# Performance work log

Hardware: AMD Instinct MI355X
Metric: run time of the kernel (lower is better)

## Reference

```python
import jax, jax.numpy as jnp
from jax import lax
import numpy as np

E = 16          # n_routed_experts
H = 2048        # hidden_size
I = 1408        # moe_intermediate_size
T = 2048        # tokens
K = 6           # top_k


def setup_inputs() -> dict:
    key = jax.random.key(0)
    k1, k2, k3, k4, k5 = jax.random.split(key, 5)
    hidden_states = jax.random.normal(k1, (T, H), dtype=jnp.float32)
    top_k_index = jax.random.randint(k2, (T, K), 0, E)
    top_k_weights = jax.random.uniform(k3, (T, K), dtype=jnp.float32)
    gate_up_proj = jax.random.normal(k4, (E, 2 * I, H), dtype=jnp.float32) * 0.02
    down_proj = jax.random.normal(k5, (E, H, I), dtype=jnp.float32) * 0.02
    return {
        "hidden_states": hidden_states,
        "top_k_index": top_k_index,
        "top_k_weights": top_k_weights,
        "gate_up_proj": gate_up_proj,
        "down_proj": down_proj,
    }


def reference(hidden_states, top_k_index, top_k_weights, gate_up_proj, down_proj):
    # combine[t, e] = sum over k-slots of top_k_weights[t, k] where top_k_index[t, k] == e
    # (scatter-add handles duplicate expert picks identically to index_add_).
    n_tok = hidden_states.shape[0]
    n_exp = gate_up_proj.shape[0]
    combine = jnp.zeros((n_tok, n_exp), hidden_states.dtype)
    combine = combine.at[jnp.arange(n_tok)[:, None], top_k_index].add(top_k_weights)

    def expert_step(acc, params):
        gu, dn, c_e = params  # gu: [2I, H], dn: [H, I], c_e: [n_tok]
        gate, up = jnp.split(hidden_states @ gu.T, 2, axis=-1)  # each [n_tok, I]
        y = (jax.nn.silu(gate) * up) @ dn.T                     # [n_tok, H]
        return acc + y * c_e[:, None], None

    out, _ = lax.scan(
        expert_step,
        jnp.zeros_like(hidden_states),
        (gate_up_proj, down_proj, combine.T),
    )
    return out
```

## Files before the change

### kernel.cpp

```cpp
#include <hip/hip_runtime.h>
#include <hip/hip_bf16.h>
#include <cstdint>

#define T_TOK 2048
#define HD 2048
#define ID 1408
#define NE 16
#define TOPK 6

#define BM 256
#define BN 64
#define BK 64

typedef __bf16 bf16x8 __attribute__((ext_vector_type(8)));
typedef float f32x4 __attribute__((ext_vector_type(4)));

typedef const __attribute__((address_space(1))) void* gas1_t;
typedef __attribute__((address_space(3))) void* las3_t;
#define GLDS16(g, l) __builtin_amdgcn_global_load_lds((gas1_t)(g), (las3_t)(l), 16, 0, 0)


__global__ void k_combine(const int* __restrict__ idx, const float* __restrict__ w,
                          float* __restrict__ combine) {
    int t = blockIdx.x * blockDim.x + threadIdx.x;
    if (t >= T_TOK) return;
    int ie[TOPK];
    float fw[TOPK];
#pragma unroll
    for (int k = 0; k < TOPK; k++) { ie[k] = idx[t * TOPK + k]; fw[k] = w[t * TOPK + k]; }
#pragma unroll
    for (int e = 0; e < NE; e++) {
        float s = 0.f;
#pragma unroll
        for (int k = 0; k < TOPK; k++) if (ie[k] == e) s += fw[k];
        combine[t * NE + e] = s;
    }
}

__global__ void k_lists(const float* __restrict__ combine, int* __restrict__ counts,
                        int* __restrict__ tok, float* __restrict__ wts) {
    int t = blockIdx.x * blockDim.x + threadIdx.x;
    if (t >= T_TOK) return;
    for (int e = 0; e < NE; e++) {
        float c = combine[t * NE + e];
        if (c != 0.0f) {
            int p = atomicAdd(&counts[e], 1);
            tok[e * T_TOK + p] = t;
            wts[e * T_TOK + p] = c;
        }
    }
}

__global__ void k_cvt(const float* __restrict__ x, __bf16* __restrict__ xb) {
    int i = (blockIdx.x * 256 + threadIdx.x) * 8;
    float4 a = *(const float4*)(x + i);
    float4 b = *(const float4*)(x + i + 4);
    bf16x8 o;
    o[0] = (__bf16)a.x; o[1] = (__bf16)a.y; o[2] = (__bf16)a.z; o[3] = (__bf16)a.w;
    o[4] = (__bf16)b.x; o[5] = (__bf16)b.y; o[6] = (__bf16)b.z; o[7] = (__bf16)b.w;
    *(bf16x8*)(xb + i) = o;
}


__device__ __forceinline__ int swz(int row, int cb) {
    return row * 128 + (cb ^ ((row & 7) << 4));
}

__device__ __forceinline__ bf16x8 ldfrag(const __bf16* base, int row, int cb) {
    return *(const bf16x8*)((const char*)base + swz(row, cb));
}

__device__ __forceinline__ void stage8v(char* lds, int row, int cb, float4 f0, float4 f1) {
    bf16x8 o;
    o[0] = (__bf16)f0.x; o[1] = (__bf16)f0.y; o[2] = (__bf16)f0.z; o[3] = (__bf16)f0.w;
    o[4] = (__bf16)f1.x; o[5] = (__bf16)f1.y; o[6] = (__bf16)f1.z; o[7] = (__bf16)f1.w;
    *(bf16x8*)(lds + swz(row, cb)) = o;
}


__global__ __launch_bounds__(512, 4) void k_gemm1(
    const __bf16* __restrict__ Xb, const float* __restrict__ gup,
    const int* __restrict__ counts, const int* __restrict__ tok,
    __bf16* __restrict__ act) {
    int x = blockIdx.x;
    int e = x / 22;
    int n0 = (x % 22) * BN;
    int cnt = counts[e];
    int m0 = blockIdx.y * BM;
    if (m0 >= cnt) return;

    __shared__ __align__(16) __bf16 sA[2][BM * BK];
    __shared__ __align__(16) __bf16 sBg[BN * BK];
    __shared__ __align__(16) __bf16 sBu[BN * BK];

    int tid = threadIdx.x;
    int lane = tid & 63;
    int wid = tid >> 6;

    const __bf16* pA[4];
    int csw = ((lane & 7) ^ ((lane >> 3) & 7)) * 8;
#pragma unroll
    for (int j = 0; j < 4; j++) {
        int r = 32 * wid + 8 * j + (lane >> 3);
        int g = m0 + r;
        if (g >= cnt) g = cnt - 1;
        pA[j] = Xb + (size_t)tok[e * T_TOK + g] * HD + csw;
    }

    int br = tid >> 3, bc = tid & 7;
    const float* gbase = gup + (size_t)e * (2 * ID) * HD;
    const float* bgSrc = gbase + (size_t)(n0 + br) * HD + bc * 8;
    const float* buSrc = gbase + (size_t)(ID + n0 + br) * HD + bc * 8;

    int wm = wid >> 1, wn = wid & 1;
    int l15 = lane & 15, lh = lane >> 4;

    f32x4 accg[4][2] = {};
    f32x4 accu[4][2] = {};

    float4 g0 = ((const float4*)bgSrc)[0], g1 = ((const float4*)bgSrc)[1];
    float4 u0 = ((const float4*)buSrc)[0], u1 = ((const float4*)buSrc)[1];
#pragma unroll
    for (int j = 0; j < 4; j++)
        GLDS16(pA[j], &sA[0][(32 * wid + 8 * j) * BK]);
    __syncthreads();

    const int NT = HD / BK;
    for (int k = 0; k < NT; k++) {
        int cur = k & 1;
        stage8v((char*)sBg, br, bc * 16, g0, g1);
        stage8v((char*)sBu, br, bc * 16, u0, u1);
        __syncthreads();

        if (k + 1 < NT) {
            int k0 = (k + 1) * BK;
#pragma unroll
            for (int j = 0; j < 4; j++)
                GLDS16(pA[j] + k0, &sA[cur ^ 1][(32 * wid + 8 * j) * BK]);
            const float* bg = bgSrc + k0;
            const float* bu = buSrc + k0;
            g0 = ((const float4*)bg)[0]; g1 = ((const float4*)bg)[1];
            u0 = ((const float4*)bu)[0]; u1 = ((const float4*)bu)[1];
        }

        const __bf16* sAc = sA[cur];
#pragma unroll
        for (int kk = 0; kk < 2; kk++) {
            int cb = kk * 64 + lh * 16;
            bf16x8 a[4];
#pragma unroll
            for (int fm = 0; fm < 4; fm++)
                a[fm] = ldfrag(sAc, wm * 64 + fm * 16 + l15, cb);
#pragma unroll
            for (int fn = 0; fn < 2; fn++) {
                bf16x8 bg = ldfrag(sBg, wn * 32 + fn * 16 + l15, cb);
                bf16x8 bu = ldfrag(sBu, wn * 32 + fn * 16 + l15, cb);
#pragma unroll
                for (int fm = 0; fm < 4; fm++) {
                    accg[fm][fn] = __builtin_amdgcn_mfma_f32_16x16x32_bf16(a[fm], bg, accg[fm][fn], 0, 0, 0);
                    accu[fm][fn] = __builtin_amdgcn_mfma_f32_16x16x32_bf16(a[fm], bu, accu[fm][fn], 0, 0, 0);
                }
            }
        }
        __syncthreads();
    }

#pragma unroll
    for (int fm = 0; fm < 4; fm++) {
#pragma unroll
        for (int fn = 0; fn < 2; fn++) {
#pragma unroll
            for (int j = 0; j < 4; j++) {
                int mloc = wm * 64 + fm * 16 + lh * 4 + j;
                int g = m0 + mloc;
                if (g < cnt) {
                    float gv = accg[fm][fn][j];
                    float uv = accu[fm][fn][j];
                    float sv = gv * (1.0f / (1.0f + __expf(-gv)));
                    int n = n0 + wn * 32 + fn * 16 + l15;
                    act[((size_t)e * T_TOK + g) * ID + n] = (__bf16)(sv * uv);
                }
            }
        }
    }
}


__global__ __launch_bounds__(512, 4) void k_gemm2(
    const __bf16* __restrict__ act, const float* __restrict__ dn,
    const int* __restrict__ counts, const int* __restrict__ tok,
    const float* __restrict__ wts, float* __restrict__ out) {
    int x = blockIdx.x;
    int e = x >> 5;
    int n0 = (x & 31) * BN;
    int cnt = counts[e];
    int m0 = blockIdx.y * BM;
    if (m0 >= cnt) return;

    __shared__ __align__(16) __bf16 sA[2][BM * BK];
    __shared__ __align__(16) __bf16 sB[BN * BK];
    __shared__ int tokLds[BM];
    __shared__ float wtLds[BM];

    int tid = threadIdx.x;
    if (tid < BM) {
        int g = m0 + tid;
        bool v = g < cnt;
        tokLds[tid] = v ? tok[e * T_TOK + g] : 0;
        wtLds[tid] = v ? wts[e * T_TOK + g] : 0.f;
    }

    int lane = tid & 63;
    int wid = tid >> 6;

    const __bf16* pA[4];
    int csw = ((lane & 7) ^ ((lane >> 3) & 7)) * 8;
#pragma unroll
    for (int j = 0; j < 4; j++) {
        int r = 32 * wid + 8 * j + (lane >> 3);
        pA[j] = act + ((size_t)e * T_TOK + m0 + r) * ID + csw;
    }

    int br = tid >> 3, bc = tid & 7;
    const float* bSrc = dn + (size_t)e * HD * ID + (size_t)(n0 + br) * ID + bc * 8;

    int wm = wid >> 1, wn = wid & 1;
    int l15 = lane & 15, lh = lane >> 4;

    f32x4 acc[4][2] = {};

    float4 b0 = ((const float4*)bSrc)[0], b1 = ((const float4*)bSrc)[1];
#pragma unroll
    for (int j = 0; j < 4; j++)
        GLDS16(pA[j], &sA[0][(32 * wid + 8 * j) * BK]);
    __syncthreads();

    const int NT = ID / BK;
    for (int k = 0; k < NT; k++) {
        int cur = k & 1;
        stage8v((char*)sB, br, bc * 16, b0, b1);
        __syncthreads();

        if (k + 1 < NT) {
            int k0 = (k + 1) * BK;
#pragma unroll
            for (int j = 0; j < 4; j++)
                GLDS16(pA[j] + k0, &sA[cur ^ 1][(32 * wid + 8 * j) * BK]);
            const float* bs = bSrc + k0;
            b0 = ((const float4*)bs)[0]; b1 = ((const float4*)bs)[1];
        }

        const __bf16* sAc = sA[cur];
#pragma unroll
        for (int kk = 0; kk < 2; kk++) {
            int cb = kk * 64 + lh * 16;
            bf16x8 a[4];
#pragma unroll
            for (int fm = 0; fm < 4; fm++)
                a[fm] = ldfrag(sAc, wm * 64 + fm * 16 + l15, cb);
#pragma unroll
            for (int fn = 0; fn < 2; fn++) {
                bf16x8 b = ldfrag(sB, wn * 32 + fn * 16 + l15, cb);
#pragma unroll
                for (int fm = 0; fm < 4; fm++)
                    acc[fm][fn] = __builtin_amdgcn_mfma_f32_16x16x32_bf16(a[fm], b, acc[fm][fn], 0, 0, 0);
            }
        }
        __syncthreads();
    }

#pragma unroll
    for (int fm = 0; fm < 4; fm++) {
#pragma unroll
        for (int fn = 0; fn < 2; fn++) {
#pragma unroll
            for (int j = 0; j < 4; j++) {
                int mloc = wm * 64 + fm * 16 + lh * 4 + j;
                int g = m0 + mloc;
                if (g < cnt) {
                    float v = acc[fm][fn][j] * wtLds[mloc];
                    int n = n0 + wn * 32 + fn * 16 + l15;
                    atomicAdd(&out[(size_t)tokLds[mloc] * HD + n], v);
                }
            }
        }
    }
}


extern "C" void kernel_launch(void* const* d_in, const int* in_sizes, int n_in,
                              void* d_out, int out_size, void* d_ws, size_t ws_size,
                              hipStream_t stream) {
    const float* hs = (const float*)d_in[0];
    const int* tki = (const int*)d_in[1];
    const float* tkw = (const float*)d_in[2];
    const float* gup = (const float*)d_in[3];
    const float* dnp = (const float*)d_in[4];
    float* out = (float*)d_out;

    char* p = (char*)d_ws;
    int* counts = (int*)p;      p += 256;
    float* combine = (float*)p; p += (size_t)T_TOK * NE * 4;
    int* tok = (int*)p;         p += (size_t)NE * T_TOK * 4;
    float* wts = (float*)p;     p += (size_t)NE * T_TOK * 4;
    __bf16* Xb = (__bf16*)p;    p += (size_t)T_TOK * HD * 2;
    __bf16* act = (__bf16*)p;

    hipMemsetAsync(counts, 0, 256, stream);
    hipMemsetAsync(d_out, 0, (size_t)T_TOK * HD * 4, stream);
    k_combine<<<T_TOK / 256, 256, 0, stream>>>(tki, tkw, combine);
    k_lists<<<T_TOK / 256, 256, 0, stream>>>(combine, counts, tok, wts);
    k_cvt<<<(T_TOK * HD / 8) / 256, 256, 0, stream>>>(hs, Xb);
    k_gemm1<<<dim3(22 * NE, T_TOK / BM), 512, 0, stream>>>(Xb, gup, counts, tok, act);
    k_gemm2<<<dim3(32 * NE, T_TOK / BM), 512, 0, stream>>>(act, dnp, counts, tok, wts, out);
}
```

Before: 471.0 us.

## Double-buffer B tiles in LDS to drop one barrier per K step

Both GEMM kernels now keep two LDS buffers for the fp32-to-bf16 staged weight tile, written for the next iteration after the MFMA loop. This removes the mid-iteration __syncthreads, leaving one barrier per K step, and hides the global B load latency behind the compute. The extra LDS raises shared memory use, and k_gemm1's launch bound drops from 4 to 2 blocks per CU, which may reduce occupancy but frees registers.

```diff
diff --git a/kernel.cpp b/kernel.cpp
--- a/kernel.cpp
+++ b/kernel.cpp
@@ -78,7 +78,7 @@
 }
 
 
-__global__ __launch_bounds__(512, 4) void k_gemm1(
+__global__ __launch_bounds__(512, 2) void k_gemm1(
     const __bf16* __restrict__ Xb, const float* __restrict__ gup,
     const int* __restrict__ counts, const int* __restrict__ tok,
     __bf16* __restrict__ act) {
@@ -90,8 +90,8 @@
     if (m0 >= cnt) return;
 
     __shared__ __align__(16) __bf16 sA[2][BM * BK];
-    __shared__ __align__(16) __bf16 sBg[BN * BK];
-    __shared__ __align__(16) __bf16 sBu[BN * BK];
+    __shared__ __align__(16) __bf16 sBg[2][BN * BK];
+    __shared__ __align__(16) __bf16 sBu[2][BN * BK];
 
     int tid = threadIdx.x;
     int lane = tid & 63;
@@ -118,25 +118,28 @@
     f32x4 accg[4][2] = {};
     f32x4 accu[4][2] = {};
 
-    float4 g0 = ((const float4*)bgSrc)[0], g1 = ((const float4*)bgSrc)[1];
-    float4 u0 = ((const float4*)buSrc)[0], u1 = ((const float4*)buSrc)[1];
-#pragma unroll
-    for (int j = 0; j < 4; j++)
-        GLDS16(pA[j], &sA[0][(32 * wid + 8 * j) * BK]);
+    const int NT = HD / BK;
+
+    {
+        float4 g0 = ((const float4*)bgSrc)[0], g1 = ((const float4*)bgSrc)[1];
+        float4 u0 = ((const float4*)buSrc)[0], u1 = ((const float4*)buSrc)[1];
+#pragma unroll
+        for (int j = 0; j < 4; j++)
+            GLDS16(pA[j], &sA[0][(32 * wid + 8 * j) * BK]);
+        stage8v((char*)sBg[0], br, bc * 16, g0, g1);
+        stage8v((char*)sBu[0], br, bc * 16, u0, u1);
+    }
     __syncthreads();
 
-    const int NT = HD / BK;
     for (int k = 0; k < NT; k++) {
-        int cur = k & 1;
-        stage8v((char*)sBg, br, bc * 16, g0, g1);
-        stage8v((char*)sBu, br, bc * 16, u0, u1);
-        __syncthreads();
-
-        if (k + 1 < NT) {
+        int cur = k & 1, nxt = cur ^ 1;
+        bool pf = (k + 1 < NT);
+        float4 g0, g1, u0, u1;
+        if (pf) {
             int k0 = (k + 1) * BK;
 #pragma unroll
             for (int j = 0; j < 4; j++)
-                GLDS16(pA[j] + k0, &sA[cur ^ 1][(32 * wid + 8 * j) * BK]);
+                GLDS16(pA[j] + k0, &sA[nxt][(32 * wid + 8 * j) * BK]);
             const float* bg = bgSrc + k0;
             const float* bu = buSrc + k0;
             g0 = ((const float4*)bg)[0]; g1 = ((const float4*)bg)[1];
@@ -144,6 +147,8 @@
         }
 
         const __bf16* sAc = sA[cur];
+        const __bf16* sBgc = sBg[cur];
+        const __bf16* sBuc = sBu[cur];
 #pragma unroll
         for (int kk = 0; kk < 2; kk++) {
             int cb = kk * 64 + lh * 16;
@@ -153,14 +158,19 @@
                 a[fm] = ldfrag(sAc, wm * 64 + fm * 16 + l15, cb);
 #pragma unroll
             for (int fn = 0; fn < 2; fn++) {
-                bf16x8 bg = ldfrag(sBg, wn * 32 + fn * 16 + l15, cb);
-                bf16x8 bu = ldfrag(sBu, wn * 32 + fn * 16 + l15, cb);
+                bf16x8 bg = ldfrag(sBgc, wn * 32 + fn * 16 + l15, cb);
+                bf16x8 bu = ldfrag(sBuc, wn * 32 + fn * 16 + l15, cb);
 #pragma unroll
                 for (int fm = 0; fm < 4; fm++) {
                     accg[fm][fn] = __builtin_amdgcn_mfma_f32_16x16x32_bf16(a[fm], bg, accg[fm][fn], 0, 0, 0);
                     accu[fm][fn] = __builtin_amdgcn_mfma_f32_16x16x32_bf16(a[fm], bu, accu[fm][fn], 0, 0, 0);
                 }
             }
+        }
+
+        if (pf) {
+            stage8v((char*)sBg[nxt], br, bc * 16, g0, g1);
+            stage8v((char*)sBu[nxt], br, bc * 16, u0, u1);
         }
         __syncthreads();
     }
@@ -198,7 +208,7 @@
     if (m0 >= cnt) return;
 
     __shared__ __align__(16) __bf16 sA[2][BM * BK];
-    __shared__ __align__(16) __bf16 sB[BN * BK];
+    __shared__ __align__(16) __bf16 sB[2][BN * BK];
     __shared__ int tokLds[BM];
     __shared__ float wtLds[BM];
 
@@ -229,28 +239,32 @@
 
     f32x4 acc[4][2] = {};
 
-    float4 b0 = ((const float4*)bSrc)[0], b1 = ((const float4*)bSrc)[1];
-#pragma unroll
-    for (int j = 0; j < 4; j++)
-        GLDS16(pA[j], &sA[0][(32 * wid + 8 * j) * BK]);
+    const int NT = ID / BK;
+
+    {
+        float4 b0 = ((const float4*)bSrc)[0], b1 = ((const float4*)bSrc)[1];
+#pragma unroll
+        for (int j = 0; j < 4; j++)
+            GLDS16(pA[j], &sA[0][(32 * wid + 8 * j) * BK]);
+        stage8v((char*)sB[0], br, bc * 16, b0, b1);
+    }
     __syncthreads();
 
-    const int NT = ID / BK;
     for (int k = 0; k < NT; k++) {
-        int cur = k & 1;
-        stage8v((char*)sB, br, bc * 16, b0, b1);
-        __syncthreads();
-
-        if (k + 1 < NT) {
+        int cur = k & 1, nxt = cur ^ 1;
+        bool pf = (k + 1 < NT);
+        float4 b0, b1;
+        if (pf) {
             int k0 = (k + 1) * BK;
 #pragma unroll
             for (int j = 0; j < 4; j++)
-                GLDS16(pA[j] + k0, &sA[cur ^ 1][(32 * wid + 8 * j) * BK]);
+                GLDS16(pA[j] + k0, &sA[nxt][(32 * wid + 8 * j) * BK]);
             const float* bs = bSrc + k0;
             b0 = ((const float4*)bs)[0]; b1 = ((const float4*)bs)[1];
         }
 
         const __bf16* sAc = sA[cur];
+        const __bf16* sBc = sB[cur];
 #pragma unroll
         for (int kk = 0; kk < 2; kk++) {
             int cb = kk * 64 + lh * 16;
@@ -260,12 +274,14 @@
                 a[fm] = ldfrag(sAc, wm * 64 + fm * 16 + l15, cb);
 #pragma unroll
             for (int fn = 0; fn < 2; fn++) {
-                bf16x8 b = ldfrag(sB, wn * 32 + fn * 16 + l15, cb);
+                bf16x8 b = ldfrag(sBc, wn * 32 + fn * 16 + l15, cb);
 #pragma unroll
                 for (int fm = 0; fm < 4; fm++)
                     acc[fm][fn] = __builtin_amdgcn_mfma_f32_16x16x32_bf16(a[fm], b, acc[fm][fn], 0, 0, 0);
             }
         }
+
+        if (pf) stage8v((char*)sB[nxt], br, bc * 16, b0, b1);
         __syncthreads();
     }
 
```

New measurement: 694.0 us. +47.4%, slower.
